# Optimization experiments

Hardware: AMD Instinct MI355X
Metric: run time of the kernel (lower is better)

The kernel has to match this reference:

```python
import jax, jax.numpy as jnp
import numpy as np

B, S, T = 256, 1024, 128

def setup_inputs() -> dict:
    key = jax.random.key(0)
    k1, k2, k3, k4, k5 = jax.random.split(key, 5)
    return {
        "emissions": jax.random.normal(k1, (B, S, T), dtype=jnp.float32),
        "tags": jax.random.randint(k2, (B, S), 0, T, dtype=jnp.int64 if jax.config.jax_enable_x64 else jnp.int32),
        "mask": jnp.ones((B, S), dtype=jnp.float32),
        "start_transitions": jax.random.normal(k3, (T,), dtype=jnp.float32),
        "end_transitions": jax.random.normal(k4, (T,), dtype=jnp.float32),
        "transitions": jax.random.normal(k5, (T, T), dtype=jnp.float32),
    }


def _gold_score(emissions, tags, mask, start_transitions, end_transitions, transitions):
    # score of the gold tag sequence (note: original uses log_softmax'd emissions here)
    score = start_transitions[tags[:, 0]]
    logp = jax.nn.log_softmax(emissions, axis=2)
    em_sc = jnp.take_along_axis(logp, tags[:, :, None], axis=2)[:, :, 0] * mask  # [B,S]
    score = score + em_sc.sum(axis=1)
    trans_sc = transitions[tags[:, :-1], tags[:, 1:]] * mask[:, 1:]  # [B,S-1]
    score = score + trans_sc.sum(axis=1)
    score = score + end_transitions[tags[:, -1]] * mask[:, -1]
    return score


def _forward_score(emissions, mask, start_transitions, end_transitions, transitions):
    # partition function via forward algorithm (faithful to original, incl. its
    # masking quirk: alpha recurrence is unmasked; only the last step's masked
    # alpha is used for the final logsumexp)
    alpha0 = start_transitions + emissions[:, 0]  # [B,T]

    def step(carry, inp):
        alpha, _ = carry
        em_t, m_t = inp  # [B,T], [B]
        # [B,T_prev,T_cur] broadcast add, logsumexp over prev tag
        new_alpha = jax.nn.logsumexp(
            alpha[:, :, None] + transitions[None, :, :] + em_t[:, None, :], axis=1
        )
        return (new_alpha, new_alpha * m_t[:, None]), None

    xs = (jnp.swapaxes(emissions[:, 1:], 0, 1), jnp.swapaxes(mask[:, 1:], 0, 1))
    (_, alpha_masked), _ = jax.lax.scan(step, (alpha0, jnp.zeros_like(alpha0)), xs)
    return jax.nn.logsumexp(alpha_masked + end_transitions, axis=1)  # [B]


def reference(emissions, tags, mask, start_transitions, end_transitions, transitions):
    score = _gold_score(emissions, tags, mask, start_transitions, end_transitions, transitions)
    fwd = _forward_score(emissions, mask, start_transitions, end_transitions, transitions)
    return jnp.mean(fwd - score)
```

## Files before the change

kernel.cpp:

```cpp
#include <hip/hip_runtime.h>

#define CRF_B 256
#define CRF_S 1024
#define CRF_T 128

typedef __attribute__((ext_vector_type(4))) float f32x4;

__device__ __forceinline__ void barrier_lds_only() {
    __asm__ volatile("s_waitcnt lgkmcnt(0)\n\ts_barrier" ::: "memory");
}

__device__ __forceinline__ float dpp_add_xor1(float x) {
    int y = __builtin_amdgcn_mov_dpp(__float_as_int(x), 0xB1, 0xF, 0xF, false);
    return x + __int_as_float(y);
}
__device__ __forceinline__ float dpp_add_xor2(float x) {
    int y = __builtin_amdgcn_mov_dpp(__float_as_int(x), 0x4E, 0xF, 0xF, false);
    return x + __int_as_float(y);
}

__device__ __forceinline__ f32x4 exp4(f32x4 v) {
    f32x4 r;
    r.x = __expf(v.x); r.y = __expf(v.y); r.z = __expf(v.z); r.w = __expf(v.w);
    return r;
}
__device__ __forceinline__ float hsum4(f32x4 v) {
    return (v.x + v.y) + (v.z + v.w);
}

__global__ __launch_bounds__(256) void crf_gold_kernel(
    const float* __restrict__ em, const int* __restrict__ tags,
    const float* __restrict__ mask, const float* __restrict__ startT,
    const float* __restrict__ endT, const float* __restrict__ trans,
    float* __restrict__ out)
{
    const int b = blockIdx.x;
    const int tid = threadIdx.x;
    const int p = tid & 3;
    const int q = tid >> 2;
    const int* tg = tags + (size_t)b * CRF_S;
    const float* mk = mask + (size_t)b * CRF_S;
    const float* emr = em + (size_t)b * CRF_S * CRF_T;

    float g_acc = 0.f;
#pragma unroll
    for (int k = 0; k < 4; ++k) {
        int t = tid + k * 256;
        int tagt = tg[t];
        float m = mk[t];
        g_acc += emr[(size_t)t * CRF_T + tagt] * m;
        if (t >= 1) g_acc += trans[tg[t - 1] * CRF_T + tagt] * m;
    }
    if (tid == 0) {
        g_acc += startT[tg[0]];
        g_acc += endT[tg[CRF_S - 1]] * mk[CRF_S - 1];
    }

    float s2 = 0.f;
#pragma unroll 1
    for (int it = 0; it < 16; ++it) {
        const int r = it * 64 + q;
        const float* row = emr + (size_t)r * CRF_T;
        f32x4 sum4 = {0.f, 0.f, 0.f, 0.f};
#pragma unroll
        for (int k = 0; k < 8; ++k)
            sum4 += exp4(*(const f32x4*)(row + k * 16 + p * 4));
        float s = hsum4(sum4);
        s = dpp_add_xor1(s);
        s = dpp_add_xor2(s);
        if (p == 0) s2 += __logf(s) * mk[r];
    }

    float contrib = s2 - g_acc;
#pragma unroll
    for (int d = 1; d < 64; d <<= 1) contrib += __shfl_xor(contrib, d);
    __shared__ float r4[4];
    if ((tid & 63) == 0) r4[tid >> 6] = contrib;
    __syncthreads();
    if (tid == 0) {
        float tot = (r4[0] + r4[1]) + (r4[2] + r4[3]);
        atomicAdd(out, tot * (1.0f / CRF_B));
    }
}

__global__ __launch_bounds__(128, 1) void crf_fwd_kernel(
    const float* __restrict__ em, const float* __restrict__ mask,
    const float* __restrict__ startT, const float* __restrict__ endT,
    const float* __restrict__ trans, float* __restrict__ out)
{
    const int b = blockIdx.x;
    const int tid = threadIdx.x;
    const int p = tid & 3;
    const int q = tid >> 2;
    const int j0 = q * 4;
    const bool leader = (p == 0);

    __shared__ __align__(16) float Abuf[2][CRF_T];
    __shared__ __align__(16) float partsA[32];
    __shared__ float red[4];
    __shared__ float lzsh;

    f32x4 EE[8][4];
#pragma unroll
    for (int k = 0; k < 8; ++k) {
        const int kp = (k + 2 * p) & 7;
#pragma unroll
        for (int s = 0; s < 4; ++s) {
            const int i = p * 32 + kp * 4 + s;
            f32x4 t4 = *(const f32x4*)&trans[i * CRF_T + j0];
            EE[k][0][s] = __expf(t4.x);
            EE[k][1][s] = __expf(t4.y);
            EE[k][2][s] = __expf(t4.z);
            EE[k][3][s] = __expf(t4.w);
        }
    }

    const float* emb = em + (size_t)b * CRF_S * CRF_T + j0;
    const float mlast = mask[(size_t)b * CRF_S + (CRF_S - 1)];

    float logZ = 0.f;
    float rc = 1.f;

    f32x4 emv[4], eh[2][4];
#pragma unroll
    for (int k = 0; k < 4; ++k) emv[k] = *(const f32x4*)(emb + (size_t)k * CRF_T);
#pragma unroll
    for (int k = 0; k < 4; ++k) eh[0][k] = exp4(emv[k]);
#pragma unroll
    for (int k = 0; k < 4; ++k) emv[k] = *(const f32x4*)(emb + (size_t)(4 + k) * CRF_T);

    auto STEP = [&](int t, int role, f32x4 ehv) {
        const int rb = (t & 1) ^ 1, wb = t & 1;

        if (role == 3 && leader) {
            const f32x4* pa = (const f32x4*)partsA;
            f32x4 s8 = ((pa[0] + pa[1]) + (pa[2] + pa[3])) +
                       ((pa[4] + pa[5]) + (pa[6] + pa[7]));
            float c = hsum4(s8);
            rc = __builtin_amdgcn_rcpf(c);
            logZ += __logf(c);
        }

        const f32x4* Ab = (const f32x4*)&Abuf[rb][p * 32];
        f32x4 ac0 = {0.f, 0.f, 0.f, 0.f}, ac1 = ac0, ac2 = ac0, ac3 = ac0;
#pragma unroll
        for (int k = 0; k < 8; ++k) {
            f32x4 av = Ab[(k + 2 * p) & 7];
            ac0 = __builtin_elementwise_fma(av, EE[k][0], ac0);
            ac1 = __builtin_elementwise_fma(av, EE[k][1], ac1);
            ac2 = __builtin_elementwise_fma(av, EE[k][2], ac2);
            ac3 = __builtin_elementwise_fma(av, EE[k][3], ac3);
        }
        float d0 = hsum4(ac0), d1 = hsum4(ac1), d2 = hsum4(ac2), d3 = hsum4(ac3);
        d0 = dpp_add_xor2(dpp_add_xor1(d0));
        d1 = dpp_add_xor2(dpp_add_xor1(d1));
        d2 = dpp_add_xor2(dpp_add_xor1(d2));
        d3 = dpp_add_xor2(dpp_add_xor1(d3));

        float a0 = d0 * ehv.x, a1 = d1 * ehv.y, a2 = d2 * ehv.z, a3 = d3 * ehv.w;
        if (role == 0) { a0 *= rc; a1 *= rc; a2 *= rc; a3 *= rc; }
        if (leader) {
            f32x4 av = {a0, a1, a2, a3};
            *(f32x4*)&Abuf[wb][j0] = av;
            if (role == 2) partsA[q] = (a0 + a1) + (a2 + a3);
        }
        barrier_lds_only();
    };

    {
        f32x4 s4 = *(const f32x4*)&startT[j0];
        if (leader) {
            f32x4 a;
            a.x = __expf(s4.x) * eh[0][0].x;
            a.y = __expf(s4.y) * eh[0][0].y;
            a.z = __expf(s4.z) * eh[0][0].z;
            a.w = __expf(s4.w) * eh[0][0].w;
            *(f32x4*)&Abuf[0][j0] = a;
        }
        barrier_lds_only();
        STEP(1, 1, eh[0][1]);
#pragma unroll
        for (int k = 0; k < 4; ++k) eh[1][k] = exp4(emv[k]);
        STEP(2, 2, eh[0][2]);
#pragma unroll
        for (int k = 0; k < 4; ++k) emv[k] = *(const f32x4*)(emb + (size_t)(8 + k) * CRF_T);
        STEP(3, 3, eh[0][3]);
    }

#pragma unroll 1
    for (int g = 1; g < 256; ++g) {
        const int t0 = 4 * g;
        const int cur = g & 1, nxt = cur ^ 1;
        STEP(t0 + 0, 0, eh[cur][0]);
        STEP(t0 + 1, 1, eh[cur][1]);
        if (g <= 254) {
#pragma unroll
            for (int k = 0; k < 4; ++k) eh[nxt][k] = exp4(emv[k]);
        }
        STEP(t0 + 2, 2, eh[cur][2]);
        if (g <= 253) {
#pragma unroll
            for (int k = 0; k < 4; ++k)
                emv[k] = *(const f32x4*)(emb + (size_t)(t0 + 8 + k) * CRF_T);
        }
        STEP(t0 + 3, 3, eh[cur][3]);
    }

    __syncthreads();
    if (tid == 0) lzsh = logZ;
    __syncthreads();
    const float lz = lzsh;

    float v = (__logf(Abuf[1][tid]) + lz) * mlast + endT[tid];
    float mx = v;
#pragma unroll
    for (int dd = 1; dd < 64; dd <<= 1) mx = fmaxf(mx, __shfl_xor(mx, dd));
    if ((tid & 63) == 0) red[tid >> 6] = mx;
    __syncthreads();
    mx = fmaxf(red[0], red[1]);
    float ex = __expf(v - mx);
#pragma unroll
    for (int dd = 1; dd < 64; dd <<= 1) ex += __shfl_xor(ex, dd);
    if ((tid & 63) == 0) red[2 + (tid >> 6)] = ex;
    __syncthreads();
    if (tid == 0) {
        float fwd = mx + __logf(red[2] + red[3]);
        atomicAdd(out, fwd * (1.0f / CRF_B));
    }
}

extern "C" void kernel_launch(void* const* d_in, const int* in_sizes, int n_in,
                              void* d_out, int out_size, void* d_ws, size_t ws_size,
                              hipStream_t stream)
{
    const float* em     = (const float*)d_in[0];
    const int*   tags   = (const int*)d_in[1];
    const float* mask   = (const float*)d_in[2];
    const float* startT = (const float*)d_in[3];
    const float* endT   = (const float*)d_in[4];
    const float* trans  = (const float*)d_in[5];
    float* out = (float*)d_out;

    hipMemsetAsync(out, 0, sizeof(float), stream);
    hipLaunchKernelGGL(crf_gold_kernel, dim3(CRF_B), dim3(256), 0, stream,
                       em, tags, mask, startT, endT, trans, out);
    hipLaunchKernelGGL(crf_fwd_kernel, dim3(CRF_B), dim3(128), 0, stream,
                       em, mask, startT, endT, trans, out);
}
```

Measured before the change: 635.4 us.

## Split forward-recurrence dot products across eight lanes with 256-thread blocks

The forward-algorithm kernel doubles its block to 256 threads, so each group of 4 output tags is served by 8 lanes instead of 4. Each lane now holds a 16x4 slice of exp(transitions) instead of 32x4, which halves the FMA chain per step. A third DPP stage (half-row mirror) completes the 8-lane reduction, and the final logsumexp is adapted to the extra waves. The aim is a shorter serial per-step latency in the sequential recurrence, at the cost of a barrier across four waves instead of two and one more cross-lane reduction step per output.

```diff
diff --git a/kernel.cpp b/kernel.cpp
--- a/kernel.cpp
+++ b/kernel.cpp
@@ -16,6 +16,10 @@
 }
 __device__ __forceinline__ float dpp_add_xor2(float x) {
     int y = __builtin_amdgcn_mov_dpp(__float_as_int(x), 0x4E, 0xF, 0xF, false);
+    return x + __int_as_float(y);
+}
+__device__ __forceinline__ float dpp_add_xor4u(float x) {
+    int y = __builtin_amdgcn_mov_dpp(__float_as_int(x), 0x141, 0xF, 0xF, false);
     return x + __int_as_float(y);
 }
 
@@ -83,30 +87,33 @@
     }
 }
 
-__global__ __launch_bounds__(128, 1) void crf_fwd_kernel(
+__global__ __launch_bounds__(256, 1) void crf_fwd_kernel(
     const float* __restrict__ em, const float* __restrict__ mask,
     const float* __restrict__ startT, const float* __restrict__ endT,
     const float* __restrict__ trans, float* __restrict__ out)
 {
     const int b = blockIdx.x;
     const int tid = threadIdx.x;
-    const int p = tid & 3;
-    const int q = tid >> 2;
-    const int j0 = q * 4;
-    const bool leader = (p == 0);
+    const int r = tid & 7;
+    const int cq = tid >> 3;
+    const int j0 = cq * 4;
+    const bool leader = (r == 0);
 
     __shared__ __align__(16) float Abuf[2][CRF_T];
     __shared__ __align__(16) float partsA[32];
-    __shared__ float red[4];
+    __shared__ float red[8];
     __shared__ float lzsh;
 
-    f32x4 EE[8][4];
-#pragma unroll
-    for (int k = 0; k < 8; ++k) {
-        const int kp = (k + 2 * p) & 7;
+    int kidx[4];
+#pragma unroll
+    for (int k = 0; k < 4; ++k) kidx[k] = (k + r) & 3;
+
+    f32x4 EE[4][4];
+#pragma unroll
+    for (int k = 0; k < 4; ++k) {
 #pragma unroll
         for (int s = 0; s < 4; ++s) {
-            const int i = p * 32 + kp * 4 + s;
+            const int i = r * 16 + kidx[k] * 4 + s;
             f32x4 t4 = *(const f32x4*)&trans[i * CRF_T + j0];
             EE[k][0][s] = __expf(t4.x);
             EE[k][1][s] = __expf(t4.y);
@@ -132,7 +139,7 @@
     auto STEP = [&](int t, int role, f32x4 ehv) {
         const int rb = (t & 1) ^ 1, wb = t & 1;
 
-        if (role == 3 && leader) {
+        if (role == 3 && leader && t < 1023) {
             const f32x4* pa = (const f32x4*)partsA;
             f32x4 s8 = ((pa[0] + pa[1]) + (pa[2] + pa[3])) +
                        ((pa[4] + pa[5]) + (pa[6] + pa[7]));
@@ -141,28 +148,28 @@
             logZ += __logf(c);
         }
 
-        const f32x4* Ab = (const f32x4*)&Abuf[rb][p * 32];
+        const f32x4* Ab = (const f32x4*)&Abuf[rb][r * 16];
         f32x4 ac0 = {0.f, 0.f, 0.f, 0.f}, ac1 = ac0, ac2 = ac0, ac3 = ac0;
 #pragma unroll
-        for (int k = 0; k < 8; ++k) {
-            f32x4 av = Ab[(k + 2 * p) & 7];
+        for (int k = 0; k < 4; ++k) {
+            f32x4 av = Ab[kidx[k]];
             ac0 = __builtin_elementwise_fma(av, EE[k][0], ac0);
             ac1 = __builtin_elementwise_fma(av, EE[k][1], ac1);
             ac2 = __builtin_elementwise_fma(av, EE[k][2], ac2);
             ac3 = __builtin_elementwise_fma(av, EE[k][3], ac3);
         }
         float d0 = hsum4(ac0), d1 = hsum4(ac1), d2 = hsum4(ac2), d3 = hsum4(ac3);
-        d0 = dpp_add_xor2(dpp_add_xor1(d0));
-        d1 = dpp_add_xor2(dpp_add_xor1(d1));
-        d2 = dpp_add_xor2(dpp_add_xor1(d2));
-        d3 = dpp_add_xor2(dpp_add_xor1(d3));
+        d0 = dpp_add_xor4u(dpp_add_xor2(dpp_add_xor1(d0)));
+        d1 = dpp_add_xor4u(dpp_add_xor2(dpp_add_xor1(d1)));
+        d2 = dpp_add_xor4u(dpp_add_xor2(dpp_add_xor1(d2)));
+        d3 = dpp_add_xor4u(dpp_add_xor2(dpp_add_xor1(d3)));
 
         float a0 = d0 * ehv.x, a1 = d1 * ehv.y, a2 = d2 * ehv.z, a3 = d3 * ehv.w;
         if (role == 0) { a0 *= rc; a1 *= rc; a2 *= rc; a3 *= rc; }
         if (leader) {
             f32x4 av = {a0, a1, a2, a3};
             *(f32x4*)&Abuf[wb][j0] = av;
-            if (role == 2) partsA[q] = (a0 + a1) + (a2 + a3);
+            if (role == 2) partsA[cq] = (a0 + a1) + (a2 + a3);
         }
         barrier_lds_only();
     };
@@ -211,20 +218,23 @@
     __syncthreads();
     const float lz = lzsh;
 
-    float v = (__logf(Abuf[1][tid]) + lz) * mlast + endT[tid];
+    float v = -3.0e38f;
+    if (tid < 128)
+        v = (__logf(Abuf[1][tid]) + lz) * mlast + endT[tid];
     float mx = v;
 #pragma unroll
     for (int dd = 1; dd < 64; dd <<= 1) mx = fmaxf(mx, __shfl_xor(mx, dd));
     if ((tid & 63) == 0) red[tid >> 6] = mx;
     __syncthreads();
-    mx = fmaxf(red[0], red[1]);
-    float ex = __expf(v - mx);
+    mx = fmaxf(fmaxf(red[0], red[1]), fmaxf(red[2], red[3]));
+    float ex = (tid < 128) ? __expf(v - mx) : 0.f;
 #pragma unroll
     for (int dd = 1; dd < 64; dd <<= 1) ex += __shfl_xor(ex, dd);
-    if ((tid & 63) == 0) red[2 + (tid >> 6)] = ex;
+    if ((tid & 63) == 0) red[4 + (tid >> 6)] = ex;
     __syncthreads();
     if (tid == 0) {
-        float fwd = mx + __logf(red[2] + red[3]);
+        float sm = (red[4] + red[5]) + (red[6] + red[7]);
+        float fwd = mx + __logf(sm);
         atomicAdd(out, fwd * (1.0f / CRF_B));
     }
 }
@@ -244,6 +254,6 @@
     hipMemsetAsync(out, 0, sizeof(float), stream);
     hipLaunchKernelGGL(crf_gold_kernel, dim3(CRF_B), dim3(256), 0, stream,
                        em, tags, mask, startT, endT, trans, out);
-    hipLaunchKernelGGL(crf_fwd_kernel, dim3(CRF_B), dim3(128), 0, stream,
+    hipLaunchKernelGGL(crf_fwd_kernel, dim3(CRF_B), dim3(256), 0, stream,
                        em, mask, startT, endT, trans, out);
 }
```

Result: faster. 598.0 us (-5.9%).
